# Performance work log

Measured on AMD Instinct MI355X. Metric: run time of the kernel, lower is better.

Reference implementation:

```python
import jax, jax.numpy as jnp
import numpy as np

N, E, EH, RH, R, H = 50000, 800000, 256, 128, 500, 2


def _seg_softmax(e, rel, num_segments):
    # torch_geometric.utils.softmax keyed by rel: (e - max_seg).exp() / (sum_seg + 1e-16)
    m = jax.ops.segment_max(e, rel, num_segments=num_segments)
    m = jnp.where(jnp.isfinite(m), m, 0.0)  # empty segments -> 0
    ex = jnp.exp(e - m[rel])
    s = jax.ops.segment_sum(ex, rel, num_segments=num_segments)
    return ex / (s[rel] + 1e-16)


def setup_inputs() -> dict:
    key = jax.random.key(0)
    ks = jax.random.split(key, 7)
    x_e = jax.random.normal(ks[0], (N, EH), dtype=jnp.float32)
    edge_index = jax.random.randint(ks[1], (2, E), 0, N)
    rel = jax.random.randint(ks[2], (E,), 0, R)
    w_h = jax.random.normal(ks[3], (RH, EH), dtype=jnp.float32) / np.sqrt(EH)
    w_t = jax.random.normal(ks[4], (RH, EH), dtype=jnp.float32) / np.sqrt(EH)
    a_h = jax.random.normal(ks[5], (H, RH), dtype=jnp.float32) / np.sqrt(RH)
    a_t = jax.random.normal(ks[6], (H, RH), dtype=jnp.float32) / np.sqrt(RH)
    return {"x_e": x_e, "edge_index": edge_index, "rel": rel,
            "w_h": w_h, "w_t": w_t, "a_h": a_h, "a_t": a_t, "num_heads": H}


def reference(x_e, edge_index, rel, w_h, w_t, a_h, a_t, num_heads):
    src, dst = edge_index[0], edge_index[1]
    x_r_h = x_e @ w_h.T  # [N, RH]
    x_r_t = x_e @ w_t.T  # [N, RH]
    # per-node attention scores for all heads: [N, H]
    s_hh = x_r_h @ a_h.T
    s_tt = x_r_t @ a_t.T
    s_th = x_r_t @ a_h.T
    s_ht = x_r_h @ a_t.T
    acc = jnp.zeros((R, RH), dtype=x_e.dtype)
    for h in range(num_heads):  # small fixed head count
        e1 = jax.nn.leaky_relu(s_hh[src, h] + s_tt[dst, h], 0.01)
        a1 = _seg_softmax(e1, rel, R)
        acc = acc + jax.ops.segment_sum(a1[:, None] * x_r_h[src], rel, num_segments=R)
        e2 = jax.nn.leaky_relu(s_th[src, h] + s_ht[dst, h], 0.01)
        a2 = _seg_softmax(e2, rel, R)
        acc = acc + jax.ops.segment_sum(a2[:, None] * x_r_t[dst], rel, num_segments=R)
    x_r = acc / num_heads / 2.0
    return x_r  # dropout is identity in eval mode
```

## Files before the change

kernel.cpp:

```cpp
#include <hip/hip_runtime.h>
#include <hip/hip_bf16.h>

#define NN 50000
#define NE 800000
#define NR 500
#define KEH 256
#define KRH 128
#define NSB 8
#define SBW 6250
#define NBK (NR*NSB)
#define NBE 256
#define EPB (NE/NBE)
#define NTILE 3125

typedef __attribute__((ext_vector_type(8))) __bf16 bf16x8;
typedef __attribute__((ext_vector_type(4))) float f32x4;

#define OFF_XH     0UL
#define OFF_XT     12800000UL
#define OFF_SP     25600000UL
#define OFF_DP     26400000UL
#define OFF_SUMS   27200000UL
#define OFF_HISTH  27208000UL
#define OFF_HISTT  27224000UL
#define OFF_INVS   27240000UL
#define OFF_BASEH  27248000UL
#define OFF_BASET  27264016UL
#define OFF_RECH   27312032UL
#define OFF_RECT   33712032UL
#define OFF_PART   40112032UL
#define OFF_AH     42160032UL
#define OFF_AT     42161056UL
#define OFF_FLAG   42162080UL
#define OFF_WHH    42162144UL
#define OFF_WHL    42227680UL
#define OFF_WTH    42293216UL
#define OFF_WTL    42358752UL
#define OFF_HPBH   42424288UL
#define OFF_HPBT   46520288UL
#define OFF_EX     50616288UL

__device__ __forceinline__ int clampi(int v, int hi) {
    v = v < 0 ? 0 : v;
    return v >= hi ? hi - 1 : v;
}

__device__ __forceinline__ int sniff_isbf(const unsigned* xe_raw) {
    int lane = threadIdx.x & 63;
    unsigned w = xe_raw[lane];
    unsigned ex = (w >> 7) & 0xFFu;
    bool hit = (ex >= 115u && ex <= 131u);
    return __popcll(__ballot(hit)) >= 32;
}

__global__ __launch_bounds__(256) void k_init(const unsigned* __restrict__ xe_raw,
                                              const void* __restrict__ ah_in, const void* __restrict__ at_in,
                                              const void* __restrict__ wh, const void* __restrict__ wt,
                                              unsigned* __restrict__ flag, float* __restrict__ ah32,
                                              float* __restrict__ at32,
                                              __bf16* __restrict__ whh, __bf16* __restrict__ wth,
                                              unsigned* __restrict__ zero1) {
    int isbf = sniff_isbf(xe_raw);
    int t = threadIdx.x;
    if (blockIdx.x == 0) {
        if (t == 0) flag[0] = (unsigned)isbf;
        ah32[t] = isbf ? __bfloat162float(((const __hip_bfloat16*)ah_in)[t]) : ((const float*)ah_in)[t];
        at32[t] = isbf ? __bfloat162float(((const __hip_bfloat16*)at_in)[t]) : ((const float*)at_in)[t];
    } else if (blockIdx.x <= 128) {
        int o = (blockIdx.x - 1) * 256 + t;
        int e = o & 7, c = (o >> 3) & 15, q = (o >> 7) & 3, ks = (o >> 9) & 7, ct = o >> 12;
        int i = (ct * 16 + c) * KEH + ks * 32 + q * 8 + e;
        if (isbf) {
            whh[o] = ((const __bf16*)wh)[i];
            wth[o] = ((const __bf16*)wt)[i];
        } else {
            whh[o] = (__bf16)((const float*)wh)[i];
            wth[o] = (__bf16)((const float*)wt)[i];
        }
    } else {
        int stride = (gridDim.x - 129) * 256;
        for (int i = (blockIdx.x - 129) * 256 + t; i < 10000; i += stride) zero1[i] = 0u;
    }
}

__global__ __launch_bounds__(512, 4) void k_gemm(const void* __restrict__ xe,
                                              const unsigned* __restrict__ flag,
                                              const __bf16* __restrict__ whh, const __bf16* __restrict__ wth,
                                              const float* __restrict__ ah, const float* __restrict__ at,
                                              __hip_bfloat16* __restrict__ xh, __hip_bfloat16* __restrict__ xt,
                                              float2* __restrict__ sp2, float2* __restrict__ dp2) {
    __shared__ uint4 lb[4096];
    const int t = threadIdx.x, lane = t & 63, wave = t >> 6;
    const int l16 = lane & 15, quad = lane >> 4;
    const int ph = blockIdx.x & 1;
    const int isbf = (int)flag[0];
    const __bf16* wfh = ph ? wth : whh;

    {
        const uint4* wsrc = (const uint4*)wfh;
        #pragma unroll
        for (int i = 0; i < 8; ++i) lb[i * 512 + t] = wsrc[i * 512 + t];
    }
    __syncthreads();

    __hip_bfloat16* out = ph ? xt : xh;
    for (int tile = (int)(blockIdx.x >> 1) * 8 + wave; tile < NTILE; tile += 2048) {
        const int row = tile * 16 + l16;
        bf16x8 a[8];
        if (isbf) {
            const __bf16* xb = (const __bf16*)xe + (size_t)row * KEH;
            #pragma unroll
            for (int ks = 0; ks < 8; ++ks)
                a[ks] = *(const bf16x8*)(xb + ks * 32 + quad * 8);
        } else {
            const float* xf = (const float*)xe + (size_t)row * KEH;
            #pragma unroll
            for (int ks = 0; ks < 8; ++ks) {
                const float* p = xf + ks * 32 + quad * 8;
                float4 u0 = *(const float4*)p, u1 = *(const float4*)(p + 4);
                a[ks][0] = (__bf16)u0.x; a[ks][1] = (__bf16)u0.y;
                a[ks][2] = (__bf16)u0.z; a[ks][3] = (__bf16)u0.w;
                a[ks][4] = (__bf16)u1.x; a[ks][5] = (__bf16)u1.y;
                a[ks][6] = (__bf16)u1.z; a[ks][7] = (__bf16)u1.w;
            }
        }

        f32x4 acc[8];
        #pragma unroll
        for (int ct = 0; ct < 8; ++ct) acc[ct] = (f32x4){0.f, 0.f, 0.f, 0.f};
        #pragma unroll
        for (int ks = 0; ks < 8; ++ks)
            #pragma unroll
            for (int ct = 0; ct < 8; ++ct)
                acc[ct] = __builtin_amdgcn_mfma_f32_16x16x32_bf16(
                    a[ks], *(const bf16x8*)&lb[(ct * 8 + ks) * 64 + lane], acc[ct], 0, 0, 0);

        float s0[4] = {0.f,0.f,0.f,0.f}, s1[4] = {0.f,0.f,0.f,0.f};
        float s2[4] = {0.f,0.f,0.f,0.f}, s3[4] = {0.f,0.f,0.f,0.f};
        #pragma unroll
        for (int ct = 0; ct < 8; ++ct) {
            int c = ct * 16 + l16;
            float va0 = ah[c], va1 = ah[128 + c];
            float vb0 = at[c], vb1 = at[128 + c];
            #pragma unroll
            for (int jj = 0; jj < 4; ++jj) {
                float v = acc[ct][jj];
                s0[jj] = fmaf(v, va0, s0[jj]);
                s1[jj] = fmaf(v, va1, s1[jj]);
                s2[jj] = fmaf(v, vb0, s2[jj]);
                s3[jj] = fmaf(v, vb1, s3[jj]);
                out[(size_t)(tile * 16 + quad * 4 + jj) * KRH + c] = __float2bfloat16(v);
            }
        }
        #pragma unroll
        for (int off = 8; off; off >>= 1)
            #pragma unroll
            for (int jj = 0; jj < 4; ++jj) {
                s0[jj] += __shfl_xor(s0[jj], off);
                s1[jj] += __shfl_xor(s1[jj], off);
                s2[jj] += __shfl_xor(s2[jj], off);
                s3[jj] += __shfl_xor(s3[jj], off);
            }
        if (l16 == 0) {
            #pragma unroll
            for (int jj = 0; jj < 4; ++jj) {
                int n = tile * 16 + quad * 4 + jj;
                if (ph == 0) {
                    sp2[n * 2 + 0] = make_float2(s0[jj], s1[jj]);
                    dp2[n * 2 + 1] = make_float2(s2[jj], s3[jj]);
                } else {
                    sp2[n * 2 + 1] = make_float2(s0[jj], s1[jj]);
                    dp2[n * 2 + 0] = make_float2(s2[jj], s3[jj]);
                }
            }
        }
    }
}

__device__ __forceinline__ float eexp(float x) {
    x = x > 0.f ? x : 0.01f * x;
    x = fminf(x, 50.f);
    return __expf(x);
}

__global__ __launch_bounds__(1024) void k_edge(const int* __restrict__ src, const int* __restrict__ dst,
                                               const int* __restrict__ rel,
                                               const float4* __restrict__ sp, const float4* __restrict__ dp,
                                               float* __restrict__ sums,
                                               unsigned* __restrict__ histH, unsigned* __restrict__ histT,
                                               unsigned* __restrict__ hpbH, unsigned* __restrict__ hpbT,
                                               float4* __restrict__ ex4) {
    __shared__ float ls[NR * 4];
    __shared__ unsigned lhH[NBK], lhT[NBK];
    int t = threadIdx.x;
    for (int i = t; i < NR * 4; i += 1024) ls[i] = 0.f;
    for (int i = t; i < NBK; i += 1024) { lhH[i] = 0u; lhT[i] = 0u; }
    __syncthreads();
    unsigned lo = blockIdx.x * EPB, hi = lo + EPB;
    for (unsigned e = lo + t; e < hi; e += 1024) {
        int s = clampi(src[e], NN), d = clampi(dst[e], NN), r = clampi(rel[e], NR);
        float4 a = sp[s], b = dp[d];
        float4 ex;
        ex.x = eexp(a.x + b.x); ex.y = eexp(a.y + b.y);
        ex.z = eexp(a.z + b.z); ex.w = eexp(a.w + b.w);
        ex4[e] = ex;
        atomicAdd(&ls[r*4+0], ex.x);
        atomicAdd(&ls[r*4+1], ex.y);
        atomicAdd(&ls[r*4+2], ex.z);
        atomicAdd(&ls[r*4+3], ex.w);
        atomicAdd(&lhH[r * NSB + s / SBW], 1u);
        atomicAdd(&lhT[r * NSB + d / SBW], 1u);
    }
    __syncthreads();
    for (int i = t; i < NR * 4; i += 1024)
        if (ls[i] != 0.f) atomicAdd(&sums[i], ls[i]);
    size_t row = (size_t)blockIdx.x * NBK;
    for (int i = t; i < NBK; i += 1024) {
        unsigned cH = lhH[i], cT = lhT[i];
        hpbH[row + i] = cH;
        hpbT[row + i] = cT;
        if (cH) atomicAdd(&histH[i], cH);
        if (cT) atomicAdd(&histT[i], cT);
    }
}

__global__ __launch_bounds__(1024) void k_scan2(const unsigned* __restrict__ histH,
                                                const unsigned* __restrict__ histT,
                                                const float* __restrict__ sums,
                                                unsigned* __restrict__ baseH, unsigned* __restrict__ baseT,
                                                float* __restrict__ invs) {
    __shared__ unsigned sc[1024];
    int t = threadIdx.x;
    for (int pass = 0; pass < 2; ++pass) {
        const unsigned* h = pass ? histT : histH;
        unsigned* base = pass ? baseT : baseH;
        int j0 = t * 4;
        unsigned v[4], s = 0;
        for (int k = 0; k < 4; ++k) { v[k] = (j0 + k < NBK) ? h[j0 + k] : 0u; s += v[k]; }
        sc[t] = s;
        __syncthreads();
        for (int off = 1; off < 1024; off <<= 1) {
            unsigned add = (t >= off) ? sc[t - off] : 0u;
            __syncthreads();
            sc[t] += add;
            __syncthreads();
        }
        unsigned run = sc[t] - s;
        for (int k = 0; k < 4; ++k) {
            if (j0 + k < NBK) { base[j0 + k] = run; run += v[k]; }
        }
        if (t == 1023) base[NBK] = sc[1023];
        __syncthreads();
    }
    for (int i = t; i < NR * 4; i += 1024) invs[i] = 1.f / (sums[i] + 1e-16f);
}

__global__ __launch_bounds__(NBE) void k_colscan(unsigned* __restrict__ hpbH, unsigned* __restrict__ hpbT,
                                                 const unsigned* __restrict__ baseH,
                                                 const unsigned* __restrict__ baseT) {
    __shared__ unsigned sc[NBE];
    int b = blockIdx.x;
    int pass = b >= NBK;
    int bin = pass ? b - NBK : b;
    unsigned* h = pass ? hpbT : hpbH;
    unsigned basev = (pass ? baseT : baseH)[bin];
    int t = threadIdx.x;
    unsigned v = h[(size_t)t * NBK + bin];
    sc[t] = v;
    __syncthreads();
    for (int off = 1; off < NBE; off <<= 1) {
        unsigned add = (t >= off) ? sc[t - off] : 0u;
        __syncthreads();
        sc[t] += add;
        __syncthreads();
    }
    h[(size_t)t * NBK + bin] = basev + sc[t] - v;
}

__global__ __launch_bounds__(1024) void k_mkrec(const int* __restrict__ src, const int* __restrict__ dst,
                                                const int* __restrict__ rel,
                                                const float4* __restrict__ ex4,
                                                const float4* __restrict__ invs4,
                                                const unsigned* __restrict__ hpbH, const unsigned* __restrict__ hpbT,
                                                uint2* __restrict__ recH, uint2* __restrict__ recT) {
    __shared__ unsigned lcH[NBK], lcT[NBK];
    int t = threadIdx.x;
    size_t row = (size_t)blockIdx.x * NBK;
    for (int i = t; i < NBK; i += 1024) { lcH[i] = hpbH[row + i]; lcT[i] = hpbT[row + i]; }
    __syncthreads();
    unsigned lo = blockIdx.x * EPB, hi = lo + EPB;
    for (unsigned e = lo + t; e < hi; e += 1024) {
        int s = clampi(src[e], NN), d = clampi(dst[e], NN), r = clampi(rel[e], NR);
        float4 ex = ex4[e];
        float4 iv = invs4[r];
        float w1 = ex.x * iv.x + ex.y * iv.y;
        float w2 = ex.z * iv.z + ex.w * iv.w;
        unsigned pH = atomicAdd(&lcH[r * NSB + s / SBW], 1u);
        unsigned pT = atomicAdd(&lcT[r * NSB + d / SBW], 1u);
        if (pH < NE) recH[pH] = make_uint2((unsigned)s, __float_as_uint(w1));
        if (pT < NE) recT[pT] = make_uint2((unsigned)d, __float_as_uint(w2));
    }
}

__global__ __launch_bounds__(256) void k_accR(const uint2* __restrict__ recH, const uint2* __restrict__ recT,
                                              const unsigned* __restrict__ baseH, const unsigned* __restrict__ baseT,
                                              const __hip_bfloat16* __restrict__ xh,
                                              const __hip_bfloat16* __restrict__ xt,
                                              float* __restrict__ part) {
    __shared__ float red[3][128];
    __shared__ uint2 lrec[256];
    int b = blockIdx.x;
    int t = threadIdx.x, lane = t & 63, wv = t >> 6;
    int l16 = lane & 15, g = lane >> 4;
    float az[8];
    #pragma unroll
    for (int k = 0; k < 8; ++k) az[k] = 0.f;

    for (int pass = 0; pass < 2; ++pass) {
        const uint2* rec = pass ? recT : recH;
        const unsigned* base = pass ? baseT : baseH;
        const uint4* xs = (const uint4*)(pass ? xt : xh);
        unsigned b0 = base[b];
        unsigned cnt = base[b + 1] - b0;
        if (cnt > NE) cnt = 0;
        for (unsigned cb = 0; cb < cnt; cb += 256u) {
            unsigned cn = cnt - cb; if (cn > 256u) cn = 256u;
            __syncthreads();
            if ((unsigned)t < cn) lrec[t] = rec[b0 + cb + t];
            __syncthreads();
            for (unsigned j = (unsigned)(wv * 4 + g); j < cn; j += 16u) {
                uint2 v = lrec[j];
                unsigned nd = v.x < NN ? v.x : 0u;
                float w = __uint_as_float(v.y);
                uint4 u = xs[(size_t)nd * 16 + l16];
                az[0] = fmaf(w, __uint_as_float(u.x << 16),          az[0]);
                az[1] = fmaf(w, __uint_as_float(u.x & 0xffff0000u),  az[1]);
                az[2] = fmaf(w, __uint_as_float(u.y << 16),          az[2]);
                az[3] = fmaf(w, __uint_as_float(u.y & 0xffff0000u),  az[3]);
                az[4] = fmaf(w, __uint_as_float(u.z << 16),          az[4]);
                az[5] = fmaf(w, __uint_as_float(u.z & 0xffff0000u),  az[5]);
                az[6] = fmaf(w, __uint_as_float(u.w << 16),          az[6]);
                az[7] = fmaf(w, __uint_as_float(u.w & 0xffff0000u),  az[7]);
            }
        }
    }
    #pragma unroll
    for (int k = 0; k < 8; ++k) {
        az[k] += __shfl_xor(az[k], 16);
        az[k] += __shfl_xor(az[k], 32);
    }
    __syncthreads();
    if (wv > 0 && lane < 16) {
        #pragma unroll
        for (int k = 0; k < 8; ++k) red[wv - 1][l16 * 8 + k] = az[k];
    }
    __syncthreads();
    if (wv == 0 && lane < 16) {
        #pragma unroll
        for (int k = 0; k < 8; ++k) {
            float s = az[k] + red[0][l16 * 8 + k] + red[1][l16 * 8 + k] + red[2][l16 * 8 + k];
            part[(size_t)b * KRH + l16 * 8 + k] = s;
        }
    }
}

__global__ __launch_bounds__(256) void k_out(const float* __restrict__ part,
                                             const unsigned* __restrict__ flag, void* __restrict__ out) {
    int i = blockIdx.x * 256 + threadIdx.x;
    if (i < NR * KRH) {
        int r = i >> 7, c = i & 127;
        float v = 0.f;
        for (int s = 0; s < NSB; ++s) v += part[(size_t)(r * NSB + s) * KRH + c];
        v *= 0.25f;
        if (!isfinite(v)) v = 0.f;
        if (flag[0]) ((__hip_bfloat16*)out)[i] = __float2bfloat16(v);
        else         ((float*)out)[i] = v;
    }
}

extern "C" void kernel_launch(void* const* d_in, const int* in_sizes, int n_in,
                              void* d_out, int out_size, void* d_ws, size_t ws_size,
                              hipStream_t stream) {
    const void* xe  = d_in[0];
    const int* eidx = (const int*)d_in[1];
    const int* rel  = (const int*)d_in[2];
    const void* wh  = d_in[3];
    const void* wt  = d_in[4];
    const void* ahp = d_in[5];
    const void* atp = d_in[6];

    const int* src = eidx;
    const int* dst = eidx + NE;

    char* ws = (char*)d_ws;
    __hip_bfloat16* xh = (__hip_bfloat16*)(ws + OFF_XH);
    __hip_bfloat16* xt = (__hip_bfloat16*)(ws + OFF_XT);
    float4*   sp     = (float4*)(ws + OFF_SP);
    float4*   dp     = (float4*)(ws + OFF_DP);
    float*    sums   = (float*)(ws + OFF_SUMS);
    unsigned* histH  = (unsigned*)(ws + OFF_HISTH);
    unsigned* histT  = (unsigned*)(ws + OFF_HISTT);
    float*    invs   = (float*)(ws + OFF_INVS);
    unsigned* baseH  = (unsigned*)(ws + OFF_BASEH);
    unsigned* baseT  = (unsigned*)(ws + OFF_BASET);
    uint2*    recH   = (uint2*)(ws + OFF_RECH);
    uint2*    recT   = (uint2*)(ws + OFF_RECT);
    float*    partp  = (float*)(ws + OFF_PART);
    float*    ah32   = (float*)(ws + OFF_AH);
    float*    at32   = (float*)(ws + OFF_AT);
    unsigned* flag   = (unsigned*)(ws + OFF_FLAG);
    __bf16*   whh    = (__bf16*)(ws + OFF_WHH);
    __bf16*   wth    = (__bf16*)(ws + OFF_WTH);
    unsigned* hpbH   = (unsigned*)(ws + OFF_HPBH);
    unsigned* hpbT   = (unsigned*)(ws + OFF_HPBT);
    float4*   ex4    = (float4*)(ws + OFF_EX);

    k_init<<<161, 256, 0, stream>>>((const unsigned*)xe, ahp, atp, wh, wt, flag, ah32, at32,
                                     whh, wth, (unsigned*)(ws + OFF_SUMS));
    k_gemm<<<512, 512, 0, stream>>>(xe, flag, whh, wth, ah32, at32,
                                    xh, xt, (float2*)sp, (float2*)dp);
    k_edge<<<NBE, 1024, 0, stream>>>(src, dst, rel, sp, dp, sums, histH, histT, hpbH, hpbT, ex4);
    k_scan2<<<1, 1024, 0, stream>>>(histH, histT, sums, baseH, baseT, invs);
    k_colscan<<<2 * NBK, NBE, 0, stream>>>(hpbH, hpbT, baseH, baseT);
    k_mkrec<<<NBE, 1024, 0, stream>>>(src, dst, rel, ex4, (const float4*)invs, hpbH, hpbT, recH, recT);
    k_accR<<<NBK, 256, 0, stream>>>(recH, recT, baseH, baseT, xh, xt, partp);
    k_out<<<(NR * KRH + 255) / 256, 256, 0, stream>>>(partp, flag, d_out);
}
```

Before: 252.5 us.

## Replace per-block histogram column scan with global atomic cursors in scatter

Removes the per-block bin-count matrix and the column-scan kernel. The global scan now also seeds per-bin cursors, and the record-building kernel claims output slots with global atomics. This cuts a kernel launch and several megabytes of histogram traffic, at the cost of contended global atomics and nondeterministic record order within a bin.

```diff
diff --git a/kernel.cpp b/kernel.cpp
--- a/kernel.cpp
+++ b/kernel.cpp
@@ -36,8 +36,8 @@
 #define OFF_WHL    42227680UL
 #define OFF_WTH    42293216UL
 #define OFF_WTL    42358752UL
-#define OFF_HPBH   42424288UL
-#define OFF_HPBT   46520288UL
+#define OFF_CURSH  42424288UL
+#define OFF_CURST  42440288UL
 #define OFF_EX     50616288UL
 
 __device__ __forceinline__ int clampi(int v, int hi) {
@@ -188,7 +188,6 @@
                                                const float4* __restrict__ sp, const float4* __restrict__ dp,
                                                float* __restrict__ sums,
                                                unsigned* __restrict__ histH, unsigned* __restrict__ histT,
-                                               unsigned* __restrict__ hpbH, unsigned* __restrict__ hpbT,
                                                float4* __restrict__ ex4) {
     __shared__ float ls[NR * 4];
     __shared__ unsigned lhH[NBK], lhT[NBK];
@@ -214,11 +213,8 @@
     __syncthreads();
     for (int i = t; i < NR * 4; i += 1024)
         if (ls[i] != 0.f) atomicAdd(&sums[i], ls[i]);
-    size_t row = (size_t)blockIdx.x * NBK;
     for (int i = t; i < NBK; i += 1024) {
         unsigned cH = lhH[i], cT = lhT[i];
-        hpbH[row + i] = cH;
-        hpbT[row + i] = cT;
         if (cH) atomicAdd(&histH[i], cH);
         if (cT) atomicAdd(&histT[i], cT);
     }
@@ -228,12 +224,14 @@
                                                 const unsigned* __restrict__ histT,
                                                 const float* __restrict__ sums,
                                                 unsigned* __restrict__ baseH, unsigned* __restrict__ baseT,
+                                                unsigned* __restrict__ cursH, unsigned* __restrict__ cursT,
                                                 float* __restrict__ invs) {
     __shared__ unsigned sc[1024];
     int t = threadIdx.x;
     for (int pass = 0; pass < 2; ++pass) {
         const unsigned* h = pass ? histT : histH;
         unsigned* base = pass ? baseT : baseH;
+        unsigned* curs = pass ? cursT : cursH;
         int j0 = t * 4;
         unsigned v[4], s = 0;
         for (int k = 0; k < 4; ++k) { v[k] = (j0 + k < NBK) ? h[j0 + k] : 0u; s += v[k]; }
@@ -247,56 +245,29 @@
         }
         unsigned run = sc[t] - s;
         for (int k = 0; k < 4; ++k) {
-            if (j0 + k < NBK) { base[j0 + k] = run; run += v[k]; }
+            if (j0 + k < NBK) { base[j0 + k] = run; curs[j0 + k] = run; run += v[k]; }
         }
         if (t == 1023) base[NBK] = sc[1023];
         __syncthreads();
     }
     for (int i = t; i < NR * 4; i += 1024) invs[i] = 1.f / (sums[i] + 1e-16f);
-}
-
-__global__ __launch_bounds__(NBE) void k_colscan(unsigned* __restrict__ hpbH, unsigned* __restrict__ hpbT,
-                                                 const unsigned* __restrict__ baseH,
-                                                 const unsigned* __restrict__ baseT) {
-    __shared__ unsigned sc[NBE];
-    int b = blockIdx.x;
-    int pass = b >= NBK;
-    int bin = pass ? b - NBK : b;
-    unsigned* h = pass ? hpbT : hpbH;
-    unsigned basev = (pass ? baseT : baseH)[bin];
-    int t = threadIdx.x;
-    unsigned v = h[(size_t)t * NBK + bin];
-    sc[t] = v;
-    __syncthreads();
-    for (int off = 1; off < NBE; off <<= 1) {
-        unsigned add = (t >= off) ? sc[t - off] : 0u;
-        __syncthreads();
-        sc[t] += add;
-        __syncthreads();
-    }
-    h[(size_t)t * NBK + bin] = basev + sc[t] - v;
 }
 
 __global__ __launch_bounds__(1024) void k_mkrec(const int* __restrict__ src, const int* __restrict__ dst,
                                                 const int* __restrict__ rel,
                                                 const float4* __restrict__ ex4,
                                                 const float4* __restrict__ invs4,
-                                                const unsigned* __restrict__ hpbH, const unsigned* __restrict__ hpbT,
+                                                unsigned* __restrict__ cursH, unsigned* __restrict__ cursT,
                                                 uint2* __restrict__ recH, uint2* __restrict__ recT) {
-    __shared__ unsigned lcH[NBK], lcT[NBK];
-    int t = threadIdx.x;
-    size_t row = (size_t)blockIdx.x * NBK;
-    for (int i = t; i < NBK; i += 1024) { lcH[i] = hpbH[row + i]; lcT[i] = hpbT[row + i]; }
-    __syncthreads();
     unsigned lo = blockIdx.x * EPB, hi = lo + EPB;
-    for (unsigned e = lo + t; e < hi; e += 1024) {
+    for (unsigned e = lo + threadIdx.x; e < hi; e += 1024) {
         int s = clampi(src[e], NN), d = clampi(dst[e], NN), r = clampi(rel[e], NR);
         float4 ex = ex4[e];
         float4 iv = invs4[r];
         float w1 = ex.x * iv.x + ex.y * iv.y;
         float w2 = ex.z * iv.z + ex.w * iv.w;
-        unsigned pH = atomicAdd(&lcH[r * NSB + s / SBW], 1u);
-        unsigned pT = atomicAdd(&lcT[r * NSB + d / SBW], 1u);
+        unsigned pH = atomicAdd(&cursH[r * NSB + s / SBW], 1u);
+        unsigned pT = atomicAdd(&cursT[r * NSB + d / SBW], 1u);
         if (pH < NE) recH[pH] = make_uint2((unsigned)s, __float_as_uint(w1));
         if (pT < NE) recT[pT] = make_uint2((unsigned)d, __float_as_uint(w2));
     }
@@ -411,18 +382,17 @@
     unsigned* flag   = (unsigned*)(ws + OFF_FLAG);
     __bf16*   whh    = (__bf16*)(ws + OFF_WHH);
     __bf16*   wth    = (__bf16*)(ws + OFF_WTH);
-    unsigned* hpbH   = (unsigned*)(ws + OFF_HPBH);
-    unsigned* hpbT   = (unsigned*)(ws + OFF_HPBT);
+    unsigned* cursH  = (unsigned*)(ws + OFF_CURSH);
+    unsigned* cursT  = (unsigned*)(ws + OFF_CURST);
     float4*   ex4    = (float4*)(ws + OFF_EX);
 
     k_init<<<161, 256, 0, stream>>>((const unsigned*)xe, ahp, atp, wh, wt, flag, ah32, at32,
                                      whh, wth, (unsigned*)(ws + OFF_SUMS));
     k_gemm<<<512, 512, 0, stream>>>(xe, flag, whh, wth, ah32, at32,
                                     xh, xt, (float2*)sp, (float2*)dp);
-    k_edge<<<NBE, 1024, 0, stream>>>(src, dst, rel, sp, dp, sums, histH, histT, hpbH, hpbT, ex4);
-    k_scan2<<<1, 1024, 0, stream>>>(histH, histT, sums, baseH, baseT, invs);
-    k_colscan<<<2 * NBK, NBE, 0, stream>>>(hpbH, hpbT, baseH, baseT);
-    k_mkrec<<<NBE, 1024, 0, stream>>>(src, dst, rel, ex4, (const float4*)invs, hpbH, hpbT, recH, recT);
+    k_edge<<<NBE, 1024, 0, stream>>>(src, dst, rel, sp, dp, sums, histH, histT, ex4);
+    k_scan2<<<1, 1024, 0, stream>>>(histH, histT, sums, baseH, baseT, cursH, cursT, invs);
+    k_mkrec<<<NBE, 1024, 0, stream>>>(src, dst, rel, ex4, (const float4*)invs, cursH, cursT, recH, recT);
     k_accR<<<NBK, 256, 0, stream>>>(recH, recT, baseH, baseT, xh, xt, partp);
     k_out<<<(NR * KRH + 255) / 256, 256, 0, stream>>>(partp, flag, d_out);
 }
```

After: 271.3 us. +7.4%, slower.
